# Performance work log

Hardware: AMD Instinct MI355X
Metric: run time of the kernel (lower is better)

The kernel has to match this reference:

```python
import jax, jax.numpy as jnp
import numpy as np

NS, NR, NT = 16, 128, 4096   # shots, receivers, time samples
NP = 100                      # quantile knots (p = linspace(0,1,100) in source)
DT = 1e-3                     # time step
FILT = 5                      # uniform_filter size for q_deriv smoothing
HP = 1.0 / (NP - 1)           # uniform p-knot spacing


def cum_trap(y, dx):
    # cumulative trapezoid along last dim, length-preserving (leading 0)
    c = jnp.cumsum(0.5 * (y[..., 1:] + y[..., :-1]), axis=-1) * dx
    return jnp.concatenate([jnp.zeros_like(y[..., :1]), c], axis=-1)


def trap(y, dx):
    return dx * (jnp.sum(y, axis=-1) - 0.5 * (y[..., 0] + y[..., -1]))


def renorm(f, dx):
    # |f| normalized to a PDF via trapezoidal rule
    a = jnp.abs(f)
    return a / trap(a, dx)[..., None]


def natural_cubic_coeffs(h, y):
    # natural cubic spline on a uniform grid; y: [..., n] -> coeffs [..., 4, n-1]
    n = y.shape[-1]
    rhs = 6.0 * (y[..., 2:] - 2.0 * y[..., 1:-1] + y[..., :-2]) / (h * h)
    A = (4.0 * jnp.eye(n - 2) + jnp.eye(n - 2, k=1) + jnp.eye(n - 2, k=-1)).astype(y.dtype)
    M_int = jnp.linalg.solve(A, rhs[..., None])[..., 0]
    M = jnp.pad(M_int, [(0, 0)] * (y.ndim - 1) + [(1, 1)])  # natural BCs: M0 = Mn-1 = 0
    a = y[..., :-1]
    b = (y[..., 1:] - y[..., :-1]) / h - h * (2.0 * M[..., :-1] + M[..., 1:]) / 6.0
    c = M[..., :-1] / 2.0
    d = (M[..., 1:] - M[..., :-1]) / (6.0 * h)
    return jnp.stack([a, b, c, d], axis=-2)


def spline_eval(coeffs, h, x, deriv=False):
    # per-trace cubic spline eval: coeffs [..., 4, n-1], x [..., m] in [0, 1]
    a, b, c, d = coeffs[..., 0, :], coeffs[..., 1, :], coeffs[..., 2, :], coeffs[..., 3, :]
    n1 = a.shape[-1]
    xi = jnp.clip(x, 0.0, n1 * h)
    idx = jnp.clip((xi / h).astype(jnp.int32), 0, n1 - 1)
    dxv = xi - idx.astype(x.dtype) * h
    g = lambda z: jnp.take_along_axis(z, idx, axis=-1)
    ai, bi, ci, di = g(a), g(b), g(c), g(d)
    if deriv:
        return bi + dxv * (2.0 * ci + 3.0 * di * dxv)
    return ai + dxv * (bi + dxv * (ci + di * dxv))


def uniform_filter1d(x, size=FILT):
    r = size // 2
    xp = jnp.pad(x, [(0, 0)] * (x.ndim - 1) + [(r, r)], mode='symmetric')
    return sum(xp[..., i:i + x.shape[-1]] for i in range(size)) / size


def build_splines(obs_data, t):
    # cts_quantile: CDF of renormalized obs, inverted at p grid, then cubic spline
    dt = t[1] - t[0]
    p = jnp.linspace(0.0, 1.0, NP, dtype=obs_data.dtype)
    F_obs = cum_trap(renorm(obs_data, dt), dt)                    # [NS,NR,NT]
    flat = F_obs.reshape(-1, F_obs.shape[-1])
    Q = jax.vmap(lambda Fi: jnp.interp(p, Fi, t))(flat)           # quantile knots
    Q = Q.reshape(*F_obs.shape[:-1], NP)
    qc = natural_cubic_coeffs(HP, Q)                              # quantile spline
    d1 = spline_eval(qc, HP, jnp.broadcast_to(p, Q.shape), deriv=True)
    d1 = uniform_filter1d(d1)                                     # filter_func
    qdc = natural_cubic_coeffs(HP, d1)                            # q_deriv spline
    return qc, qdc


def setup_inputs() -> dict:
    key = jax.random.key(0)
    k1, k2 = jax.random.split(key)
    f = jax.random.normal(k1, (NS, NR, NT), dtype=jnp.float32)
    obs_data = jax.random.normal(k2, (NS, NR, NT), dtype=jnp.float32)
    t = jnp.arange(NT, dtype=jnp.float32) * DT
    return {"f": f, "obs_data": obs_data, "t": t}


def reference(f, obs_data, t):
    dt = t[1] - t[0]
    qc, _ = build_splines(obs_data, t)
    f_tilde = renorm(f, dt)
    F = cum_trap(f_tilde, dt)                    # per-trace CDF, values in [0,1]
    off_diag = spline_eval(qc, HP, F)            # Q_obs(F(t)) spline gather
    diff = t - off_diag
    integrated = trap(diff * diff * f_tilde, dt)
    return integrated.sum()
```

## Files before the change

kernel.cpp:

```cpp
#include <hip/hip_runtime.h>

#define NS 16
#define NR 128
#define NT 4096
#define NPP 100
#define NROWS (NS * NR)
#define BLK 256
#define EPT 16

__global__ __launch_bounds__(BLK) void wass_row_kernel(
    const float* __restrict__ f, const float* __restrict__ obs,
    float* __restrict__ rowOut) {
  const int row  = blockIdx.x;
  const int tid  = threadIdx.x;
  const int lane = tid & 63;
  const int wid  = tid >> 6;

  __shared__ float sF[NT];
  __shared__ float sQ[NPP];
  __shared__ float sM[NPP];
  __shared__ float sRhs[NPP];
  __shared__ float sCp[NPP];
  __shared__ float sDp[NPP];
  __shared__ float sA[NPP], sB[NPP], sC[NPP], sD[NPP];
  __shared__ float sWave[4];
  __shared__ float sWaveOff[4];
  __shared__ float sTot, sY0, sYlast;

  const float hF   = (float)(1.0 / 99.0);
  const float hhF  = (float)((1.0 / 99.0) * (1.0 / 99.0));
  const float sixh = (float)(6.0 * (1.0 / 99.0));

  float y[EPT];
  {
    const float4* op = (const float4*)(obs + (size_t)row * NT);
#pragma unroll
    for (int q = 0; q < 4; ++q) {
      float4 v = op[tid * 4 + q];
      y[4 * q + 0] = fabsf(v.x);
      y[4 * q + 1] = fabsf(v.y);
      y[4 * q + 2] = fabsf(v.z);
      y[4 * q + 3] = fabsf(v.w);
    }
  }
  float localSum = 0.f;
#pragma unroll
  for (int j = 0; j < EPT; ++j) localSum += y[j];

  float v = localSum;
#pragma unroll
  for (int off = 1; off < 64; off <<= 1) {
    float n = __shfl_up(v, off, 64);
    if (lane >= off) v += n;
  }
  if (lane == 63) sWave[wid] = v;
  if (tid == 0) sY0 = y[0];
  if (tid == BLK - 1) sYlast = y[EPT - 1];
  __syncthreads();
  if (tid == 0) {
    float acc = 0.f;
#pragma unroll
    for (int w2 = 0; w2 < 4; ++w2) { sWaveOff[w2] = acc; acc += sWave[w2]; }
    sTot = acc;
  }
  __syncthreads();
  {
    float threadExcl = (v - localSum) + sWaveOff[wid];
    float y0   = sY0;
    float Traw = sTot - 0.5f * (sY0 + sYlast);
    float invT = 1.0f / Traw;
    float ex = threadExcl;
    int base = tid * EPT;
#pragma unroll
    for (int j = 0; j < EPT; ++j) {
      sF[base + j] = (ex + 0.5f * (y[j] - y0)) * invT;
      ex += y[j];
    }
  }
  __syncthreads();

  if (tid < NPP) {
    float x = (float)((double)tid * (1.0 / 99.0));
    int lo = 0, hi = NT;
    while (lo < hi) {
      int mid = (lo + hi) >> 1;
      if (sF[mid] > x) hi = mid; else lo = mid + 1;
    }
    int i = lo;
    if (i < 1) i = 1;
    if (i > NT - 1) i = NT - 1;
    float Fj = sF[i - 1], Fi = sF[i];
    float dxv = Fi - Fj;
    float tj = (float)(i - 1) * 0.001f;
    float ti = (float)i * 0.001f;
    float qv = (dxv == 0.0f) ? ti : tj + ((x - Fj) / dxv) * (ti - tj);
    sQ[tid] = qv;
  }
  __syncthreads();

  if (tid < NPP - 2) {
    sRhs[tid] = 6.0f * (sQ[tid + 2] - 2.0f * sQ[tid + 1] + sQ[tid]) / hhF;
  }
  __syncthreads();

  if (tid == 0) {
    float cp_prev = 0.f, dp_prev = 0.f;
    for (int i = 0; i < NPP - 2; ++i) {
      float m  = 4.0f - cp_prev;
      float ci = 1.0f / m;
      float di = (sRhs[i] - dp_prev) * ci;
      sCp[i] = ci; sDp[i] = di;
      cp_prev = ci; dp_prev = di;
    }
    float Mi = sDp[NPP - 3];
    sM[NPP - 2] = Mi;
    for (int i = NPP - 4; i >= 0; --i) {
      Mi = sDp[i] - sCp[i] * Mi;
      sM[i + 1] = Mi;
    }
    sM[0] = 0.f;
    sM[NPP - 1] = 0.f;
  }
  __syncthreads();

  if (tid < NPP - 1) {
    float yi = sQ[tid], yi1 = sQ[tid + 1];
    float Mi = sM[tid], Mi1 = sM[tid + 1];
    sA[tid] = yi;
    sB[tid] = (yi1 - yi) / hF - hF * (2.0f * Mi + Mi1) / 6.0f;
    sC[tid] = 0.5f * Mi;
    sD[tid] = (Mi1 - Mi) / sixh;
  }
  __syncthreads();

  {
    const float4* fp4 = (const float4*)(f + (size_t)row * NT);
#pragma unroll
    for (int q = 0; q < 4; ++q) {
      float4 vv = fp4[tid * 4 + q];
      y[4 * q + 0] = fabsf(vv.x);
      y[4 * q + 1] = fabsf(vv.y);
      y[4 * q + 2] = fabsf(vv.z);
      y[4 * q + 3] = fabsf(vv.w);
    }
  }
  localSum = 0.f;
#pragma unroll
  for (int j = 0; j < EPT; ++j) localSum += y[j];

  v = localSum;
#pragma unroll
  for (int off = 1; off < 64; off <<= 1) {
    float n = __shfl_up(v, off, 64);
    if (lane >= off) v += n;
  }
  if (lane == 63) sWave[wid] = v;
  if (tid == 0) sY0 = y[0];
  if (tid == BLK - 1) sYlast = y[EPT - 1];
  __syncthreads();
  if (tid == 0) {
    float acc = 0.f;
#pragma unroll
    for (int w2 = 0; w2 < 4; ++w2) { sWaveOff[w2] = acc; acc += sWave[w2]; }
    sTot = acc;
  }
  __syncthreads();

  float acc = 0.f;
  float TrawF;
  {
    float threadExcl = (v - localSum) + sWaveOff[wid];
    float y0 = sY0;
    TrawF = sTot - 0.5f * (sY0 + sYlast);
    float invT = 1.0f / TrawF;
    float ex = threadExcl;
    int base = tid * EPT;
#pragma unroll
    for (int j = 0; j < EPT; ++j) {
      int k = base + j;
      float yv = y[j];
      float Fk = (ex + 0.5f * (yv - y0)) * invT;
      ex += yv;
      float xi = Fk;
      if (xi < 0.0f) xi = 0.0f;
      if (xi > 1.0f) xi = 1.0f;
      int idx = (int)(xi / hF);
      if (idx > NPP - 2) idx = NPP - 2;
      float dxv = xi - (float)idx * hF;
      float val = sA[idx] + dxv * (sB[idx] + dxv * (sC[idx] + dxv * sD[idx]));
      float tk = (float)k * 0.001f;
      float diff = tk - val;
      float w = (k == 0 || k == NT - 1) ? 0.5f : 1.0f;
      acc += w * diff * diff * yv;
    }
  }

#pragma unroll
  for (int off = 32; off > 0; off >>= 1) acc += __shfl_down(acc, off, 64);
  if (lane == 0) sWave[wid] = acc;
  __syncthreads();
  if (tid == 0) {
    float s = sWave[0] + sWave[1] + sWave[2] + sWave[3];
    rowOut[row] = s / TrawF;
  }
}

__global__ __launch_bounds__(256) void wass_reduce_kernel(
    const float* __restrict__ rowOut, float* __restrict__ out) {
  __shared__ double sW[4];
  int tid = threadIdx.x;
  int lane = tid & 63, wid = tid >> 6;
  double acc = 0.0;
  for (int i = tid; i < NROWS; i += 256) acc += (double)rowOut[i];
#pragma unroll
  for (int off = 32; off > 0; off >>= 1) acc += __shfl_down(acc, off, 64);
  if (lane == 0) sW[wid] = acc;
  __syncthreads();
  if (tid == 0) out[0] = (float)(sW[0] + sW[1] + sW[2] + sW[3]);
}

extern "C" void kernel_launch(void* const* d_in, const int* in_sizes, int n_in,
                              void* d_out, int out_size, void* d_ws, size_t ws_size,
                              hipStream_t stream) {
  (void)in_sizes; (void)n_in; (void)out_size; (void)ws_size;
  const float* f   = (const float*)d_in[0];
  const float* obs = (const float*)d_in[1];
  float* rowOut = (float*)d_ws;

  wass_row_kernel<<<NROWS, BLK, 0, stream>>>(f, obs, rowOut);
  wass_reduce_kernel<<<1, 256, 0, stream>>>(rowOut, (float*)d_out);
}
```

Baseline: 107.8 us.

## Parallelize tridiagonal solve via cyclic reduction and scatter quantiles from CDF segments

Replaces the serial single-thread Thomas solve for the spline second derivatives with a parallel cyclic-reduction scheme over 98 threads. It also replaces the per-knot binary search over a shared CDF array by having each thread scatter the quantile knots that fall inside its own CDF segments, so the 16 KB shared CDF buffer goes away. Both obs and f are loaded and prefix-scanned together to overlap memory latency and share barriers. Spline coefficients are packed as float4 for a single shared-memory load. Cyclic reduction does more arithmetic and may differ slightly numerically from the sequential solve.

After: 141.0 us. 30.8% more time.

```diff
diff --git a/kernel.cpp b/kernel.cpp
--- a/kernel.cpp
+++ b/kernel.cpp
@@ -1,12 +1,16 @@
 #include <hip/hip_runtime.h>
 
-#define NS 16
-#define NR 128
 #define NT 4096
 #define NPP 100
-#define NROWS (NS * NR)
+#define NROWS 2048
 #define BLK 256
 #define EPT 16
+#define NM 98
+#define DTIME 0.001f
+
+__device__ __forceinline__ float pgrid(int k) {
+  return (float)((double)k * (1.0 / 99.0));
+}
 
 __global__ __launch_bounds__(BLK) void wass_row_kernel(
     const float* __restrict__ f, const float* __restrict__ obs,
@@ -16,179 +20,172 @@
   const int lane = tid & 63;
   const int wid  = tid >> 6;
 
-  __shared__ float sF[NT];
   __shared__ float sQ[NPP];
   __shared__ float sM[NPP];
-  __shared__ float sRhs[NPP];
-  __shared__ float sCp[NPP];
-  __shared__ float sDp[NPP];
-  __shared__ float sA[NPP], sB[NPP], sC[NPP], sD[NPP];
-  __shared__ float sWave[4];
-  __shared__ float sWaveOff[4];
-  __shared__ float sTot, sY0, sYlast;
-
-  const float hF   = (float)(1.0 / 99.0);
-  const float hhF  = (float)((1.0 / 99.0) * (1.0 / 99.0));
-  const float sixh = (float)(6.0 * (1.0 / 99.0));
-
-  float y[EPT];
+  __shared__ float4 sCo[NPP - 1];
+  __shared__ float sPa[2][NM], sPb[2][NM], sPc[2][NM], sPd[2][NM];
+  __shared__ float sFlast[BLK];
+  __shared__ float sWo[4], sWf[4], sWoOff[4], sWfOff[4];
+  __shared__ float sTotO, sTotF, sY0o, sYlo, sY0f, sYlf;
+
+  float yo[EPT], yf[EPT];
   {
     const float4* op = (const float4*)(obs + (size_t)row * NT);
+    const float4* fp = (const float4*)(f + (size_t)row * NT);
+    float4 vo[4], vf[4];
+#pragma unroll
+    for (int q = 0; q < 4; ++q) vo[q] = op[tid * 4 + q];
+#pragma unroll
+    for (int q = 0; q < 4; ++q) vf[q] = fp[tid * 4 + q];
 #pragma unroll
     for (int q = 0; q < 4; ++q) {
-      float4 v = op[tid * 4 + q];
-      y[4 * q + 0] = fabsf(v.x);
-      y[4 * q + 1] = fabsf(v.y);
-      y[4 * q + 2] = fabsf(v.z);
-      y[4 * q + 3] = fabsf(v.w);
-    }
-  }
-  float localSum = 0.f;
-#pragma unroll
-  for (int j = 0; j < EPT; ++j) localSum += y[j];
-
-  float v = localSum;
+      yo[4*q+0] = fabsf(vo[q].x); yo[4*q+1] = fabsf(vo[q].y);
+      yo[4*q+2] = fabsf(vo[q].z); yo[4*q+3] = fabsf(vo[q].w);
+      yf[4*q+0] = fabsf(vf[q].x); yf[4*q+1] = fabsf(vf[q].y);
+      yf[4*q+2] = fabsf(vf[q].z); yf[4*q+3] = fabsf(vf[q].w);
+    }
+  }
+
+  float so = 0.f, sf = 0.f;
+#pragma unroll
+  for (int j = 0; j < EPT; ++j) { so += yo[j]; sf += yf[j]; }
+  float vo = so, vf = sf;
 #pragma unroll
   for (int off = 1; off < 64; off <<= 1) {
-    float n = __shfl_up(v, off, 64);
-    if (lane >= off) v += n;
-  }
-  if (lane == 63) sWave[wid] = v;
-  if (tid == 0) sY0 = y[0];
-  if (tid == BLK - 1) sYlast = y[EPT - 1];
+    float no = __shfl_up(vo, off, 64);
+    float nf = __shfl_up(vf, off, 64);
+    if (lane >= off) { vo += no; vf += nf; }
+  }
+  if (lane == 63) { sWo[wid] = vo; sWf[wid] = vf; }
+  if (tid == 0)       { sY0o = yo[0];       sY0f = yf[0]; }
+  if (tid == BLK - 1) { sYlo = yo[EPT - 1]; sYlf = yf[EPT - 1]; }
   __syncthreads();
   if (tid == 0) {
-    float acc = 0.f;
-#pragma unroll
-    for (int w2 = 0; w2 < 4; ++w2) { sWaveOff[w2] = acc; acc += sWave[w2]; }
-    sTot = acc;
-  }
-  __syncthreads();
+    float a = 0.f, b = 0.f;
+#pragma unroll
+    for (int w = 0; w < 4; ++w) {
+      sWoOff[w] = a; a += sWo[w];
+      sWfOff[w] = b; b += sWf[w];
+    }
+    sTotO = a; sTotF = b;
+  }
+  __syncthreads();
+
+  const float exO  = (vo - so) + sWoOff[wid];
+  const float exF  = (vf - sf) + sWfOff[wid];
+  const float y0o  = sY0o;
+  const float TrO  = sTotO - 0.5f * (sY0o + sYlo);
+  const float invTO = 1.0f / TrO;
+
+  sFlast[tid] = (exO + so - yo[EPT-1] + 0.5f * (yo[EPT-1] - y0o)) * invTO;
+  __syncthreads();
+
   {
-    float threadExcl = (v - localSum) + sWaveOff[wid];
-    float y0   = sY0;
-    float Traw = sTot - 0.5f * (sY0 + sYlast);
-    float invT = 1.0f / Traw;
-    float ex = threadExcl;
+    float aPrev = (tid == 0) ? 0.0f : sFlast[tid - 1];
+    float ex = exO;
     int base = tid * EPT;
 #pragma unroll
     for (int j = 0; j < EPT; ++j) {
-      sF[base + j] = (ex + 0.5f * (y[j] - y0)) * invT;
-      ex += y[j];
-    }
-  }
-  __syncthreads();
-
-  if (tid < NPP) {
-    float x = (float)((double)tid * (1.0 / 99.0));
-    int lo = 0, hi = NT;
-    while (lo < hi) {
-      int mid = (lo + hi) >> 1;
-      if (sF[mid] > x) hi = mid; else lo = mid + 1;
-    }
-    int i = lo;
-    if (i < 1) i = 1;
-    if (i > NT - 1) i = NT - 1;
-    float Fj = sF[i - 1], Fi = sF[i];
-    float dxv = Fi - Fj;
-    float tj = (float)(i - 1) * 0.001f;
-    float ti = (float)i * 0.001f;
-    float qv = (dxv == 0.0f) ? ti : tj + ((x - Fj) / dxv) * (ti - tj);
-    sQ[tid] = qv;
-  }
-  __syncthreads();
-
-  if (tid < NPP - 2) {
-    sRhs[tid] = 6.0f * (sQ[tid + 2] - 2.0f * sQ[tid + 1] + sQ[tid]) / hhF;
-  }
-  __syncthreads();
-
-  if (tid == 0) {
-    float cp_prev = 0.f, dp_prev = 0.f;
-    for (int i = 0; i < NPP - 2; ++i) {
-      float m  = 4.0f - cp_prev;
-      float ci = 1.0f / m;
-      float di = (sRhs[i] - dp_prev) * ci;
-      sCp[i] = ci; sDp[i] = di;
-      cp_prev = ci; dp_prev = di;
-    }
-    float Mi = sDp[NPP - 3];
-    sM[NPP - 2] = Mi;
-    for (int i = NPP - 4; i >= 0; --i) {
-      Mi = sDp[i] - sCp[i] * Mi;
-      sM[i + 1] = Mi;
-    }
-    sM[0] = 0.f;
-    sM[NPP - 1] = 0.f;
-  }
+      int k0 = base + j;
+      float b = (ex + 0.5f * (yo[j] - y0o)) * invTO;
+      ex += yo[j];
+      if (k0 == 0) {
+        sQ[0] = 0.0f;
+      } else {
+        float a = aPrev;
+        int kLo = (int)floorf(a * 99.0f);
+        if (kLo < 0) kLo = 0;
+        while (kLo > 0 && pgrid(kLo - 1) > a) --kLo;
+        while (kLo <= 99 && pgrid(kLo) <= a) ++kLo;
+        int kHi = (int)floorf(b * 99.0f) + 1;
+        if (kHi > 99) kHi = 99;
+        while (kHi >= 0 && pgrid(kHi) > b) --kHi;
+        if (k0 == NT - 1) kHi = 99;
+        float tPrev = (float)(k0 - 1) * DTIME;
+        float denom = b - a;
+        for (int k = kLo; k <= kHi; ++k) {
+          float r = (denom > 0.f) ? (pgrid(k) - a) / denom : 1.0f;
+          sQ[k] = tPrev + r * DTIME;
+        }
+      }
+      aPrev = b;
+    }
+  }
+  __syncthreads();
+
+  int pp = 0;
+  if (tid < NM) {
+    float rhs = 6.0f * 99.0f * 99.0f * (sQ[tid + 2] - 2.0f * sQ[tid + 1] + sQ[tid]);
+    sPa[0][tid] = (tid == 0)      ? 0.f : 1.f;
+    sPb[0][tid] = 4.f;
+    sPc[0][tid] = (tid == NM - 1) ? 0.f : 1.f;
+    sPd[0][tid] = rhs;
+  }
+  __syncthreads();
+
+  for (int s = 1; s < NM; s <<= 1) {
+    if (tid < NM) {
+      float ai = sPa[pp][tid], bi = sPb[pp][tid];
+      float ci = sPc[pp][tid], di = sPd[pp][tid];
+      float alpha = 0.f, am = 0.f, cm = 0.f, dm = 0.f;
+      int im = tid - s;
+      if (im >= 0) {
+        float bm = sPb[pp][im];
+        am = sPa[pp][im]; cm = sPc[pp][im]; dm = sPd[pp][im];
+        alpha = -ai / bm;
+      }
+      float gamma = 0.f, ap = 0.f, cp2 = 0.f, dp2 = 0.f;
+      int ip = tid + s;
+      if (ip < NM) {
+        float bp = sPb[pp][ip];
+        ap = sPa[pp][ip]; cp2 = sPc[pp][ip]; dp2 = sPd[pp][ip];
+        gamma = -ci / bp;
+      }
+      sPa[1 - pp][tid] = alpha * am;
+      sPc[1 - pp][tid] = gamma * cp2;
+      sPb[1 - pp][tid] = bi + alpha * cm + gamma * ap;
+      sPd[1 - pp][tid] = di + alpha * dm + gamma * dp2;
+    }
+    pp ^= 1;
+    __syncthreads();
+  }
+
+  if (tid < NM) sM[tid + 1] = sPd[pp][tid] / sPb[pp][tid];
+  if (tid == NM) { sM[0] = 0.f; sM[NPP - 1] = 0.f; }
   __syncthreads();
 
   if (tid < NPP - 1) {
     float yi = sQ[tid], yi1 = sQ[tid + 1];
     float Mi = sM[tid], Mi1 = sM[tid + 1];
-    sA[tid] = yi;
-    sB[tid] = (yi1 - yi) / hF - hF * (2.0f * Mi + Mi1) / 6.0f;
-    sC[tid] = 0.5f * Mi;
-    sD[tid] = (Mi1 - Mi) / sixh;
-  }
-  __syncthreads();
-
+    float4 co;
+    co.x = yi;
+    co.y = (yi1 - yi) * 99.0f - (1.0f / 99.0f) * (2.0f * Mi + Mi1) * (1.0f / 6.0f);
+    co.z = 0.5f * Mi;
+    co.w = (Mi1 - Mi) * (99.0f / 6.0f);
+    sCo[tid] = co;
+  }
+  __syncthreads();
+
+  const float y0f  = sY0f;
+  const float TrF  = sTotF - 0.5f * (sY0f + sYlf);
+  const float invTF = 1.0f / TrF;
+  float acc = 0.f;
   {
-    const float4* fp4 = (const float4*)(f + (size_t)row * NT);
-#pragma unroll
-    for (int q = 0; q < 4; ++q) {
-      float4 vv = fp4[tid * 4 + q];
-      y[4 * q + 0] = fabsf(vv.x);
-      y[4 * q + 1] = fabsf(vv.y);
-      y[4 * q + 2] = fabsf(vv.z);
-      y[4 * q + 3] = fabsf(vv.w);
-    }
-  }
-  localSum = 0.f;
-#pragma unroll
-  for (int j = 0; j < EPT; ++j) localSum += y[j];
-
-  v = localSum;
-#pragma unroll
-  for (int off = 1; off < 64; off <<= 1) {
-    float n = __shfl_up(v, off, 64);
-    if (lane >= off) v += n;
-  }
-  if (lane == 63) sWave[wid] = v;
-  if (tid == 0) sY0 = y[0];
-  if (tid == BLK - 1) sYlast = y[EPT - 1];
-  __syncthreads();
-  if (tid == 0) {
-    float acc = 0.f;
-#pragma unroll
-    for (int w2 = 0; w2 < 4; ++w2) { sWaveOff[w2] = acc; acc += sWave[w2]; }
-    sTot = acc;
-  }
-  __syncthreads();
-
-  float acc = 0.f;
-  float TrawF;
-  {
-    float threadExcl = (v - localSum) + sWaveOff[wid];
-    float y0 = sY0;
-    TrawF = sTot - 0.5f * (sY0 + sYlast);
-    float invT = 1.0f / TrawF;
-    float ex = threadExcl;
+    float ex = exF;
     int base = tid * EPT;
 #pragma unroll
     for (int j = 0; j < EPT; ++j) {
       int k = base + j;
-      float yv = y[j];
-      float Fk = (ex + 0.5f * (yv - y0)) * invT;
+      float yv = yf[j];
+      float Fk = (ex + 0.5f * (yv - y0f)) * invTF;
       ex += yv;
-      float xi = Fk;
-      if (xi < 0.0f) xi = 0.0f;
-      if (xi > 1.0f) xi = 1.0f;
-      int idx = (int)(xi / hF);
+      float xi = fminf(fmaxf(Fk, 0.f), 1.f);
+      int idx = (int)(xi * 99.0f);
       if (idx > NPP - 2) idx = NPP - 2;
-      float dxv = xi - (float)idx * hF;
-      float val = sA[idx] + dxv * (sB[idx] + dxv * (sC[idx] + dxv * sD[idx]));
-      float tk = (float)k * 0.001f;
+      float dxv = xi - (float)idx * (1.0f / 99.0f);
+      float4 co = sCo[idx];
+      float val = co.x + dxv * (co.y + dxv * (co.z + dxv * co.w));
+      float tk = (float)k * DTIME;
       float diff = tk - val;
       float w = (k == 0 || k == NT - 1) ? 0.5f : 1.0f;
       acc += w * diff * diff * yv;
@@ -197,11 +194,10 @@
 
 #pragma unroll
   for (int off = 32; off > 0; off >>= 1) acc += __shfl_down(acc, off, 64);
-  if (lane == 0) sWave[wid] = acc;
+  if (lane == 0) sWo[wid] = acc;
   __syncthreads();
   if (tid == 0) {
-    float s = sWave[0] + sWave[1] + sWave[2] + sWave[3];
-    rowOut[row] = s / TrawF;
+    rowOut[row] = (sWo[0] + sWo[1] + sWo[2] + sWo[3]) * invTF;
   }
 }
 
```
